# Optimization experiments

Measured on AMD Instinct MI355X. Metric: run time of the kernel, lower is better.

## Reference

```python
import jax, jax.numpy as jnp
import numpy as np

N, D, E = 100000, 128, 600000  # nodes, feature dim, edges
EPS = 1e-5  # BatchNorm1d default eps


def setup_inputs() -> dict:
    key = jax.random.key(0)
    k = jax.random.split(key, 4)
    x = jax.random.normal(k[0], (N, D), jnp.float32)
    edge_index = jax.random.randint(k[1], (2, E), 0, N, jnp.int32)  # [src; dst]
    W = jax.random.normal(k[2], (D, D), jnp.float32) * (1.0 / np.sqrt(D))
    b = jnp.zeros((D,), jnp.float32)
    gamma = jnp.ones((D,), jnp.float32)
    beta = jnp.zeros((D,), jnp.float32)
    return dict(x=x, edge_index=edge_index, W=W, b=b, gamma=gamma, beta=beta)


def reference(x, edge_index, W, b, gamma, beta):
    # dropout p=0 -> identity
    src, dst = edge_index[0], edge_index[1]
    ones = jnp.ones((E,), x.dtype)
    deg_out = jnp.maximum(jax.ops.segment_sum(ones, src, num_segments=N), 1.0)
    deg_in = jnp.maximum(jax.ops.segment_sum(ones, dst, num_segments=N), 1.0)
    # GraphConv norm='both': D_out^{-1/2} on src side, sum-aggregate, D_in^{-1/2} on dst side
    h = x * jax.lax.rsqrt(deg_out)[:, None]            # [N, D]
    agg = jax.ops.segment_sum(h[src], dst, num_segments=N)  # gather+scatter over edges
    agg = agg * jax.lax.rsqrt(deg_in)[:, None]
    new_x = agg @ W + b                                 # linear after aggregation
    # residual (num_dst_nodes == N for a homogeneous graph)
    h = x + new_x
    # BatchNorm1d, training-mode batch statistics (biased variance)
    mean = jnp.mean(h, axis=0)
    var = jnp.var(h, axis=0)
    h = (h - mean) * jax.lax.rsqrt(var + EPS) * gamma + beta
    return jax.nn.relu(h)
```

## Files before the change

### kernel.cpp

```cpp
#include <hip/hip_runtime.h>
#include <math.h>

#define D 128
#define NGB 512
#define SLOTS 32
#define WB 8
#define XB 512
#define RANGES 16
#define BPR 64
constexpr float EPS = 1e-5f;

typedef short v8s __attribute__((ext_vector_type(8)));
typedef float v4f __attribute__((ext_vector_type(4)));

__device__ __forceinline__ unsigned short f2bf(float f) {
    union { float f; unsigned u; } c; c.f = f;
    unsigned u = c.u;
    return (unsigned short)((u + 0x7FFFu + ((u >> 16) & 1u)) >> 16);
}
__device__ __forceinline__ float bf2f(unsigned short u) {
    union { unsigned u; float f; } c; c.u = ((unsigned)u) << 16; return c.f;
}

__global__ void prep_kernel(const int* __restrict__ src, const int* __restrict__ dst,
                            const float* __restrict__ W, const float4* __restrict__ x4,
                            int* __restrict__ deg_in, int* __restrict__ esrc,
                            unsigned short* __restrict__ wfrag, ushort4* __restrict__ xb4,
                            unsigned short* __restrict__ degpart,
                            int n, int E, int total4, int GB, int CHv) {
    __shared__ int hist[6400];
    const int bid = blockIdx.x;
    const int tid = threadIdx.x;
    if (bid < GB) {
        int e = bid * 256 + tid;
        if (e < E) {
            int s = src[e], d = dst[e];
            int pos = atomicAdd(&deg_in[d], 1);
            if (pos < SLOTS) esrc[((size_t)d << 5) | pos] = s;
        }
    } else if (bid < GB + WB) {
        int t = (bid - GB) * 256 + tid;
        int lane = t & 63;
        int nt = (t >> 6) & 7;
        int kt = t >> 9;
        int col = nt * 16 + (lane & 15);
        int k0 = kt * 32 + (lane >> 4) * 8;
        unsigned short* dstp = wfrag + (size_t)t * 8;
        #pragma unroll
        for (int j = 0; j < 8; ++j) dstp[j] = f2bf(W[(size_t)(k0 + j) * D + col]);
    } else if (bid < GB + WB + XB) {
        for (int f = (bid - GB - WB) * 256 + tid; f < total4; f += XB * 256) {
            float4 v = x4[f];
            ushort4 o;
            o.x = f2bf(v.x); o.y = f2bf(v.y); o.z = f2bf(v.z); o.w = f2bf(v.w);
            xb4[f] = o;
        }
    } else {
        const int h = bid - (GB + WB + XB);
        const int r = h / BPR;
        const int sub = h - r * BPR;
        const int base = r * CHv;
        for (int i = tid; i < CHv; i += 256) hist[i] = 0;
        __syncthreads();
        const int per = (E + BPR - 1) / BPR;
        const int e0 = sub * per;
        const int e1 = min(e0 + per, E);
        for (int e = e0 + tid; e < e1; e += 256) {
            int u = src[e] - base;
            if ((unsigned)u < (unsigned)CHv) atomicAdd(&hist[u], 1);
        }
        __syncthreads();
        unsigned short* outp = degpart + (size_t)h * CHv;
        for (int i = tid; i < CHv; i += 256) outp[i] = (unsigned short)hist[i];
    }
}

__global__ void rsdeg_kernel(const unsigned short* __restrict__ degpart,
                             float* __restrict__ rs_out, int n, int CHv) {
    int v = blockIdx.x * blockDim.x + threadIdx.x;
    if (v < n) {
        int r = v / CHv, u = v - r * CHv;
        const unsigned short* p = degpart + ((size_t)r * BPR) * CHv + u;
        int s = 0;
        #pragma unroll
        for (int k = 0; k < BPR; ++k) s += p[(size_t)k * CHv];
        rs_out[v] = rsqrtf(fmaxf((float)s, 1.0f));
    }
}

__global__ __launch_bounds__(256)
void agg_kernel(const ushort4* __restrict__ xb4, const float* __restrict__ rs_out,
                const int* __restrict__ deg_in, const int* __restrict__ esrc,
                ushort4* __restrict__ aggb4, int n) {
    int g = blockIdx.x * 8 + (threadIdx.x >> 5);
    int l32 = threadIdx.x & 31;
    if (g >= n) return;
    int deg = deg_in[g];
    int cnt = min(deg, SLOTS);
    int sE = (l32 < cnt) ? esrc[((size_t)g << 5) + l32] : 0;
    float rv = (l32 < cnt) ? rs_out[sE] : 0.f;
    float4 acc = make_float4(0.f, 0.f, 0.f, 0.f);
    int e = 0;
    for (; e + 3 < cnt; e += 4) {
        int s0 = __shfl(sE, e, 32),     s1 = __shfl(sE, e + 1, 32);
        int s2 = __shfl(sE, e + 2, 32), s3 = __shfl(sE, e + 3, 32);
        float c0 = __shfl(rv, e, 32),     c1 = __shfl(rv, e + 1, 32);
        float c2 = __shfl(rv, e + 2, 32), c3 = __shfl(rv, e + 3, 32);
        ushort4 u0 = xb4[(size_t)s0 * 32 + l32];
        ushort4 u1 = xb4[(size_t)s1 * 32 + l32];
        ushort4 u2 = xb4[(size_t)s2 * 32 + l32];
        ushort4 u3 = xb4[(size_t)s3 * 32 + l32];
        acc.x += bf2f(u0.x) * c0 + bf2f(u1.x) * c1 + bf2f(u2.x) * c2 + bf2f(u3.x) * c3;
        acc.y += bf2f(u0.y) * c0 + bf2f(u1.y) * c1 + bf2f(u2.y) * c2 + bf2f(u3.y) * c3;
        acc.z += bf2f(u0.z) * c0 + bf2f(u1.z) * c1 + bf2f(u2.z) * c2 + bf2f(u3.z) * c3;
        acc.w += bf2f(u0.w) * c0 + bf2f(u1.w) * c1 + bf2f(u2.w) * c2 + bf2f(u3.w) * c3;
    }
    for (; e < cnt; ++e) {
        int s0 = __shfl(sE, e, 32);
        float c0 = __shfl(rv, e, 32);
        ushort4 u0 = xb4[(size_t)s0 * 32 + l32];
        acc.x += bf2f(u0.x) * c0;
        acc.y += bf2f(u0.y) * c0;
        acc.z += bf2f(u0.z) * c0;
        acc.w += bf2f(u0.w) * c0;
    }
    float si = rsqrtf(fmaxf((float)deg, 1.0f));
    ushort4 o;
    o.x = f2bf(acc.x * si);
    o.y = f2bf(acc.y * si);
    o.z = f2bf(acc.z * si);
    o.w = f2bf(acc.w * si);
    aggb4[(size_t)g * 32 + l32] = o;
}

__global__ __launch_bounds__(256, 4)
void gemm_mfma_kernel(const v8s* __restrict__ aggb8,
                      const v8s* __restrict__ wfrag8,
                      const float* __restrict__ b,
                      const float* __restrict__ x,
                      float* __restrict__ out,
                      float* __restrict__ bnpart, int n) {
    const int lane = threadIdx.x & 63;
    const int wave = threadIdx.x >> 6;
    const int half = wave & 1;
    const int wpair = wave >> 1;
    const int gpair = blockIdx.x * 2 + wpair;
    const int npairs = gridDim.x * 2;
    const int ntiles = (n + 15) >> 4;
    const int c = lane & 15;
    const int s = lane >> 4;

    v8s wf[4][4];
    #pragma unroll
    for (int kt = 0; kt < 4; ++kt)
        #pragma unroll
        for (int nt = 0; nt < 4; ++nt)
            wf[kt][nt] = wfrag8[(kt * 8 + half * 4 + nt) * 64 + lane];

    float bv[4];
    #pragma unroll
    for (int nt = 0; nt < 4; ++nt) bv[nt] = b[(half * 4 + nt) * 16 + c];

    float hs[4], hq[4];
    #pragma unroll
    for (int nt = 0; nt < 4; ++nt) { hs[nt] = 0.f; hq[nt] = 0.f; }

    for (int tile = gpair; tile < ntiles; tile += npairs) {
        const int row0 = tile * 16;
        int arow = row0 + c;
        if (arow >= n) arow = n - 1;

        v4f acc[4];
        #pragma unroll
        for (int nt = 0; nt < 4; ++nt) acc[nt] = (v4f)(0.f);

        #pragma unroll
        for (int kt = 0; kt < 4; ++kt) {
            v8s af = aggb8[(size_t)arow * 16 + kt * 4 + s];
            #pragma unroll
            for (int nt = 0; nt < 4; ++nt)
                acc[nt] = __builtin_amdgcn_mfma_f32_16x16x32_bf16(af, wf[kt][nt], acc[nt], 0, 0, 0);
        }

        #pragma unroll
        for (int j = 0; j < 4; ++j) {
            int m = row0 + s * 4 + j;
            if (m < n) {
                const float* xr = x + (size_t)m * D;
                float* orow = out + (size_t)m * D;
                #pragma unroll
                for (int nt = 0; nt < 4; ++nt) {
                    int col = (half * 4 + nt) * 16 + c;
                    float h = acc[nt][j] + bv[nt] + xr[col];
                    orow[col] = h;
                    hs[nt] += h;
                    hq[nt] += h * h;
                }
            }
        }
    }

    #pragma unroll
    for (int nt = 0; nt < 4; ++nt) {
        hs[nt] += __shfl_xor(hs[nt], 16); hs[nt] += __shfl_xor(hs[nt], 32);
        hq[nt] += __shfl_xor(hq[nt], 16); hq[nt] += __shfl_xor(hq[nt], 32);
    }
    __shared__ float ls[4][64];
    __shared__ float lq[4][64];
    if (s == 0) {
        #pragma unroll
        for (int nt = 0; nt < 4; ++nt) {
            ls[wave][nt * 16 + c] = hs[nt];
            lq[wave][nt * 16 + c] = hq[nt];
        }
    }
    __syncthreads();
    const int t = threadIdx.x;
    if (t < 128) {
        int hh = t >> 6, ii = t & 63;
        bnpart[(size_t)t * NGB + blockIdx.x] = ls[hh][ii] + ls[hh + 2][ii];
    } else {
        int cc = t - 128;
        int hh = cc >> 6, ii = cc & 63;
        bnpart[(size_t)(128 + cc) * NGB + blockIdx.x] = lq[hh][ii] + lq[hh + 2][ii];
    }
}

__global__ __launch_bounds__(256)
void stats_params_kernel(const float* __restrict__ partial, const float* __restrict__ gamma,
                         const float* __restrict__ beta, float* __restrict__ scale,
                         float* __restrict__ shift, float inv_n) {
    const int col = blockIdx.x;
    const int t = threadIdx.x;
    float a = partial[(size_t)col * NGB + t] + partial[(size_t)col * NGB + 256 + t];
    float q = partial[(size_t)(128 + col) * NGB + t] + partial[(size_t)(128 + col) * NGB + 256 + t];
    #pragma unroll
    for (int off = 32; off >= 1; off >>= 1) {
        a += __shfl_xor(a, off);
        q += __shfl_xor(q, off);
    }
    __shared__ float wa[4], wq[4];
    if ((t & 63) == 0) { wa[t >> 6] = a; wq[t >> 6] = q; }
    __syncthreads();
    if (t == 0) {
        float sum = wa[0] + wa[1] + wa[2] + wa[3];
        float sq  = wq[0] + wq[1] + wq[2] + wq[3];
        float mean = sum * inv_n;
        float var = fmaxf(sq * inv_n - mean * mean, 0.f);
        float inv = rsqrtf(var + EPS);
        float sc = gamma[col] * inv;
        scale[col] = sc;
        shift[col] = beta[col] - mean * sc;
    }
}

__global__ void final_kernel(float4* __restrict__ h4, const float4* __restrict__ scale4,
                             const float4* __restrict__ shift4, int total4) {
    int stride = gridDim.x * blockDim.x;
    for (int f = blockIdx.x * blockDim.x + threadIdx.x; f < total4; f += stride) {
        int c4 = f & 31;
        float4 v = h4[f];
        float4 s = scale4[c4];
        float4 sh = shift4[c4];
        float4 r;
        r.x = fmaxf(fmaf(v.x, s.x, sh.x), 0.f);
        r.y = fmaxf(fmaf(v.y, s.y, sh.y), 0.f);
        r.z = fmaxf(fmaf(v.z, s.z, sh.z), 0.f);
        r.w = fmaxf(fmaf(v.w, s.w, sh.w), 0.f);
        h4[f] = r;
    }
}

extern "C" void kernel_launch(void* const* d_in, const int* in_sizes, int n_in,
                              void* d_out, int out_size, void* d_ws, size_t ws_size,
                              hipStream_t stream) {
    const float* x     = (const float*)d_in[0];
    const int*   ei    = (const int*)d_in[1];
    const float* W     = (const float*)d_in[2];
    const float* b     = (const float*)d_in[3];
    const float* gamma = (const float*)d_in[4];
    const float* beta  = (const float*)d_in[5];

    const int E = in_sizes[1] / 2;
    const int n = in_sizes[0] / D;
    const int* src = ei;
    const int* dst = ei + E;

    const int CHv = (n + RANGES - 1) / RANGES;
    const int GB = (E + 255) / 256;
    const int HB = RANGES * BPR;

    unsigned short* xb    = (unsigned short*)d_ws;
    unsigned short* aggb  = xb + (size_t)n * D;
    unsigned short* wfrag = aggb + (size_t)n * D;
    int*   deg_in   = (int*)(wfrag + 2048 * 8);
    float* rs_out   = (float*)(deg_in + n);
    float* scale    = rs_out + n;
    float* shift    = scale + 128;
    float* bnpart   = shift + 128;

    int* esrc = (int*)d_out;
    unsigned short* degpart = (unsigned short*)(esrc + (size_t)n * SLOTS);

    hipMemsetAsync(deg_in, 0, (size_t)n * sizeof(int), stream);

    prep_kernel<<<GB + WB + XB + HB, 256, 0, stream>>>(src, dst, W, (const float4*)x,
                                                       deg_in, esrc, wfrag, (ushort4*)xb,
                                                       degpart, n, E, n * 32, GB, CHv);
    rsdeg_kernel<<<(n + 255) / 256, 256, 0, stream>>>(degpart, rs_out, n, CHv);
    agg_kernel<<<(n + 7) / 8, 256, 0, stream>>>((const ushort4*)xb, rs_out, deg_in, esrc,
                                                (ushort4*)aggb, n);
    gemm_mfma_kernel<<<NGB, 256, 0, stream>>>((const v8s*)aggb, (const v8s*)wfrag,
                                              b, x, (float*)d_out, bnpart, n);
    stats_params_kernel<<<128, 256, 0, stream>>>(bnpart, gamma, beta, scale, shift,
                                                 1.0f / (float)n);
    final_kernel<<<4096, 256, 0, stream>>>((float4*)d_out, (const float4*)scale,
                                           (const float4*)shift, n * 32);
}
```

Baseline: 136.6 us.

## Replace global-atomic dst bucketing with LDS histogram, scan, and deterministic bucket pass

Building the per-destination edge list no longer uses one global atomicAdd per edge on deg_in. Each edge chunk now builds an LDS histogram of dst counts per node range, and a scan kernel turns these into per-chunk slot offsets, deg_in and the src-degree rsqrt. A second bucketing kernel then fills esrc slots with LDS atomics. This removes the global memset and contended global atomics but adds an extra pass over the edge arrays and another kernel launch.

```diff
diff --git a/kernel.cpp b/kernel.cpp
--- a/kernel.cpp
+++ b/kernel.cpp
@@ -24,22 +24,42 @@
 
 __global__ void prep_kernel(const int* __restrict__ src, const int* __restrict__ dst,
                             const float* __restrict__ W, const float4* __restrict__ x4,
-                            int* __restrict__ deg_in, int* __restrict__ esrc,
+                            unsigned short* __restrict__ hcnt_src,
+                            unsigned short* __restrict__ hcnt_dst,
                             unsigned short* __restrict__ wfrag, ushort4* __restrict__ xb4,
-                            unsigned short* __restrict__ degpart,
-                            int n, int E, int total4, int GB, int CHv) {
+                            int n, int E, int total4, int CHv) {
     __shared__ int hist[6400];
     const int bid = blockIdx.x;
     const int tid = threadIdx.x;
-    if (bid < GB) {
-        int e = bid * 256 + tid;
-        if (e < E) {
-            int s = src[e], d = dst[e];
-            int pos = atomicAdd(&deg_in[d], 1);
-            if (pos < SLOTS) esrc[((size_t)d << 5) | pos] = s;
-        }
-    } else if (bid < GB + WB) {
-        int t = (bid - GB) * 256 + tid;
+    const int HB = RANGES * BPR;
+    if (bid < 2 * HB) {
+        const int isDst = (bid >= HB);
+        const int h = isDst ? bid - HB : bid;
+        const int r = h / BPR;
+        const int sub = h - r * BPR;
+        const int base = r * CHv;
+        const int* arr = isDst ? dst : src;
+        for (int i = tid; i < CHv; i += 256) hist[i] = 0;
+        __syncthreads();
+        const int per = (E + BPR - 1) / BPR;
+        const int e0 = sub * per;
+        const int e1 = min(e0 + per, E);
+        for (int e = e0 + tid; e < e1; e += 256) {
+            int u = arr[e] - base;
+            if ((unsigned)u < (unsigned)CHv) atomicAdd(&hist[u], 1);
+        }
+        __syncthreads();
+        unsigned short* outp = (isDst ? hcnt_dst : hcnt_src) + (size_t)h * CHv;
+        for (int i = tid; i < CHv; i += 256) outp[i] = (unsigned short)hist[i];
+    } else if (bid < 2 * HB + XB) {
+        for (int f = (bid - 2 * HB) * 256 + tid; f < total4; f += XB * 256) {
+            float4 v = x4[f];
+            ushort4 o;
+            o.x = f2bf(v.x); o.y = f2bf(v.y); o.z = f2bf(v.z); o.w = f2bf(v.w);
+            xb4[f] = o;
+        }
+    } else {
+        int t = (bid - 2 * HB - XB) * 256 + tid;
         int lane = t & 63;
         int nt = (t >> 6) & 7;
         int kt = t >> 9;
@@ -48,43 +68,75 @@
         unsigned short* dstp = wfrag + (size_t)t * 8;
         #pragma unroll
         for (int j = 0; j < 8; ++j) dstp[j] = f2bf(W[(size_t)(k0 + j) * D + col]);
-    } else if (bid < GB + WB + XB) {
-        for (int f = (bid - GB - WB) * 256 + tid; f < total4; f += XB * 256) {
-            float4 v = x4[f];
-            ushort4 o;
-            o.x = f2bf(v.x); o.y = f2bf(v.y); o.z = f2bf(v.z); o.w = f2bf(v.w);
-            xb4[f] = o;
-        }
-    } else {
-        const int h = bid - (GB + WB + XB);
-        const int r = h / BPR;
-        const int sub = h - r * BPR;
-        const int base = r * CHv;
-        for (int i = tid; i < CHv; i += 256) hist[i] = 0;
-        __syncthreads();
-        const int per = (E + BPR - 1) / BPR;
-        const int e0 = sub * per;
-        const int e1 = min(e0 + per, E);
-        for (int e = e0 + tid; e < e1; e += 256) {
-            int u = src[e] - base;
-            if ((unsigned)u < (unsigned)CHv) atomicAdd(&hist[u], 1);
-        }
-        __syncthreads();
-        unsigned short* outp = degpart + (size_t)h * CHv;
-        for (int i = tid; i < CHv; i += 256) outp[i] = (unsigned short)hist[i];
-    }
-}
-
-__global__ void rsdeg_kernel(const unsigned short* __restrict__ degpart,
-                             float* __restrict__ rs_out, int n, int CHv) {
-    int v = blockIdx.x * blockDim.x + threadIdx.x;
-    if (v < n) {
-        int r = v / CHv, u = v - r * CHv;
-        const unsigned short* p = degpart + ((size_t)r * BPR) * CHv + u;
-        int s = 0;
-        #pragma unroll
-        for (int k = 0; k < BPR; ++k) s += p[(size_t)k * CHv];
-        rs_out[v] = rsqrtf(fmaxf((float)s, 1.0f));
+    }
+}
+
+__global__ __launch_bounds__(256)
+void scan_kernel(const unsigned short* __restrict__ hcnt_src,
+                 const unsigned short* __restrict__ hcnt_dst,
+                 unsigned short* __restrict__ sbase, int* __restrict__ deg_in,
+                 float* __restrict__ rs_out, int n, int CHv) {
+    __shared__ int pc[4][64];
+    __shared__ int psrc[4][64];
+    const int tid = threadIdx.x;
+    const int nl = tid & 63;
+    const int c = tid >> 6;
+    const int v = blockIdx.x * 64 + nl;
+    const bool ok = (v < n);
+    int r = 0, u = 0;
+    if (ok) { r = v / CHv; u = v - r * CHv; }
+
+    unsigned short tmp[16];
+    int sum16 = 0, ssum = 0;
+    if (ok) {
+        const unsigned short* pd = hcnt_dst + ((size_t)(r * BPR + c * 16)) * CHv + u;
+        #pragma unroll
+        for (int j = 0; j < 16; ++j) { tmp[j] = pd[(size_t)j * CHv]; sum16 += tmp[j]; }
+        const unsigned short* ps = hcnt_src + ((size_t)(r * BPR + c * 16)) * CHv + u;
+        #pragma unroll
+        for (int j = 0; j < 16; ++j) ssum += ps[(size_t)j * CHv];
+    }
+    pc[c][nl] = sum16;
+    psrc[c][nl] = ssum;
+    __syncthreads();
+    if (ok) {
+        int run = 0;
+        #pragma unroll
+        for (int cc = 0; cc < 4; ++cc) if (cc < c) run += pc[cc][nl];
+        unsigned short* sbp = sbase + ((size_t)(r * BPR + c * 16)) * CHv + u;
+        #pragma unroll
+        for (int j = 0; j < 16; ++j) { sbp[(size_t)j * CHv] = (unsigned short)run; run += tmp[j]; }
+        if (c == 3) deg_in[v] = run;
+        if (c == 0) {
+            int tot = psrc[0][nl] + psrc[1][nl] + psrc[2][nl] + psrc[3][nl];
+            rs_out[v] = rsqrtf(fmaxf((float)tot, 1.0f));
+        }
+    }
+}
+
+__global__ __launch_bounds__(256)
+void bucket2_kernel(const int* __restrict__ src, const int* __restrict__ dst,
+                    const unsigned short* __restrict__ sbase, int* __restrict__ esrc,
+                    int E, int CHv) {
+    __shared__ int lh[6400];
+    const int tid = threadIdx.x;
+    const int h = blockIdx.x;
+    const int r = h / BPR;
+    const int sub = h - r * BPR;
+    const int base = r * CHv;
+    const unsigned short* sbp = sbase + (size_t)h * CHv;
+    for (int i = tid; i < CHv; i += 256) lh[i] = sbp[i];
+    __syncthreads();
+    const int per = (E + BPR - 1) / BPR;
+    const int e0 = sub * per;
+    const int e1 = min(e0 + per, E);
+    for (int e = e0 + tid; e < e1; e += 256) {
+        int d = dst[e];
+        int u = d - base;
+        if ((unsigned)u < (unsigned)CHv) {
+            int slot = atomicAdd(&lh[u], 1);
+            if (slot < SLOTS) esrc[((size_t)d << 5) | slot] = src[e];
+        }
     }
 }
 
@@ -287,7 +339,6 @@
     const int* dst = ei + E;
 
     const int CHv = (n + RANGES - 1) / RANGES;
-    const int GB = (E + 255) / 256;
     const int HB = RANGES * BPR;
 
     unsigned short* xb    = (unsigned short*)d_ws;
@@ -300,14 +351,16 @@
     float* bnpart   = shift + 128;
 
     int* esrc = (int*)d_out;
-    unsigned short* degpart = (unsigned short*)(esrc + (size_t)n * SLOTS);
-
-    hipMemsetAsync(deg_in, 0, (size_t)n * sizeof(int), stream);
-
-    prep_kernel<<<GB + WB + XB + HB, 256, 0, stream>>>(src, dst, W, (const float4*)x,
-                                                       deg_in, esrc, wfrag, (ushort4*)xb,
-                                                       degpart, n, E, n * 32, GB, CHv);
-    rsdeg_kernel<<<(n + 255) / 256, 256, 0, stream>>>(degpart, rs_out, n, CHv);
+    unsigned short* hcnt_src = (unsigned short*)(esrc + (size_t)n * SLOTS);
+    unsigned short* hcnt_dst = hcnt_src + (size_t)HB * CHv;
+    unsigned short* sbase    = hcnt_dst + (size_t)HB * CHv;
+
+    prep_kernel<<<2 * HB + XB + WB, 256, 0, stream>>>(src, dst, W, (const float4*)x,
+                                                      hcnt_src, hcnt_dst, wfrag,
+                                                      (ushort4*)xb, n, E, n * 32, CHv);
+    scan_kernel<<<(n + 63) / 64, 256, 0, stream>>>(hcnt_src, hcnt_dst, sbase, deg_in,
+                                                   rs_out, n, CHv);
+    bucket2_kernel<<<HB, 256, 0, stream>>>(src, dst, sbase, esrc, E, CHv);
     agg_kernel<<<(n + 7) / 8, 256, 0, stream>>>((const ushort4*)xb, rs_out, deg_in, esrc,
                                                 (ushort4*)aggb, n);
     gemm_mfma_kernel<<<NGB, 256, 0, stream>>>((const v8s*)aggb, (const v8s*)wfrag,
```

Result: slower. 148.0 us (+8.3%).
